# Optimization experiments

Measured on AMD Instinct MI355X. Metric: run time of the kernel, lower is better.

## Reference

```python
import jax, jax.numpy as jnp
import numpy as np

N, DIN, H, NCLS = 1024, 128, 64, 40
NEG = -1e30  # stand-in for -inf in masked max (grad-safe)


def _linw(k, fan_in, fan_out):
    s = 1.0 / np.sqrt(fan_in)
    return jax.random.uniform(k, (fan_in, fan_out), jnp.float32, -s, s)


def setup_inputs() -> dict:
    key = jax.random.key(0)
    ks = jax.random.split(key, 10)
    x = jax.random.normal(ks[0], (N, DIN), jnp.float32)
    A = jax.random.bernoulli(ks[1], 0.05, (N, N))  # bool adjacency
    D2 = 2 * H  # layer output width (concat self || neigh)
    return {
        "x": x, "A": A,
        # layer 1 (in=DIN)
        "Wp1": _linw(ks[2], DIN, DIN), "bp1": jnp.zeros((DIN,), jnp.float32),
        "Ws1": _linw(ks[3], DIN, H),   "bs1": jnp.zeros((H,), jnp.float32),
        "Wn1": _linw(ks[4], DIN, H),   "bn1": jnp.zeros((H,), jnp.float32),
        # layer 2 (in=2*H)
        "Wp2": _linw(ks[5], D2, D2),   "bp2": jnp.zeros((D2,), jnp.float32),
        "Ws2": _linw(ks[6], D2, H),    "bs2": jnp.zeros((H,), jnp.float32),
        "Wn2": _linw(ks[7], D2, H),    "bn2": jnp.zeros((H,), jnp.float32),
        # head
        "Wh": _linw(ks[8], D2, NCLS),  "bh": jnp.zeros((NCLS,), jnp.float32),
    }


def _sage_layer(x, A, Wp, bp, Ws, bs, Wn, bn):
    # maxpool aggregator: relu(Linear_pool(x_u)), elementwise max over neighbors u of v
    pooled = jax.nn.relu(x @ Wp + bp)                                  # [N, Din]
    agg = jnp.max(jnp.where(A[:, :, None], pooled[None, :, :], NEG), axis=1)  # [N, Din]
    agg = jnp.where(agg <= NEG * 0.5, 0.0, agg)                        # isolated nodes -> 0
    # out_channels = 2*hidden: concat(self transform, neighbor transform)
    return jnp.concatenate([x @ Ws + bs, agg @ Wn + bn], axis=-1)      # [N, 2H]


def _block(x, A, Wp, bp, Ws, bs, Wn, bn):
    h = jax.nn.relu(_sage_layer(x, A, Wp, bp, Ws, bs, Wn, bn))
    nrm = jnp.maximum(jnp.linalg.norm(h, axis=-1, keepdims=True), 1e-12)
    return h / nrm


def reference(x, A, Wp1, bp1, Ws1, bs1, Wn1, bn1,
              Wp2, bp2, Ws2, bs2, Wn2, bn2, Wh, bh):
    h = _block(x, A, Wp1, bp1, Ws1, bs1, Wn1, bn1)
    h = _block(h, A, Wp2, bp2, Ws2, bs2, Wn2, bn2)
    return h @ Wh + bh  # [N, n_classes]
```

## Files before the change

kernel.cpp:

```cpp
#include <hip/hip_runtime.h>

#define NN 1024

__global__ __launch_bounds__(512) void lin_build(
    const float* __restrict__ X, const float* __restrict__ Wp,
    const float* __restrict__ bp, const float* __restrict__ Ws,
    const float* __restrict__ bs, const int* __restrict__ A,
    float* __restrict__ pooled, float* __restrict__ sbuf,
    int* __restrict__ nbrG, int* __restrict__ cntG)
{
    __shared__ float xL[4][128];
    __shared__ float lp[2][4][192];
    __shared__ unsigned long long masksL[4][16];
    __shared__ int pfxL[4][16];

    const int tid  = threadIdx.x;
    const int lane = tid & 63;
    const int wv   = tid >> 6;
    const int v0   = blockIdx.x * 4;

    xL[tid >> 7][tid & 127] = X[v0 * 128 + tid];
    __syncthreads();

    if (tid < 384) {
        const int kh = (tid >= 192) ? 1 : 0;
        const int j = tid - kh * 192;
        const float* w; int ld;
        if (j < 128) { w = Wp + j;         ld = 128; }
        else         { w = Ws + (j - 128); ld = 64;  }
        const int k0 = kh * 64;
        float a0 = 0.f, a1 = 0.f, a2 = 0.f, a3 = 0.f;
        #pragma unroll 4
        for (int k = 0; k < 64; ++k) {
            const float wvv = w[(k0 + k) * ld];
            a0 += xL[0][k0 + k] * wvv;  a1 += xL[1][k0 + k] * wvv;
            a2 += xL[2][k0 + k] * wvv;  a3 += xL[3][k0 + k] * wvv;
        }
        lp[kh][0][j] = a0; lp[kh][1][j] = a1; lp[kh][2][j] = a2; lp[kh][3][j] = a3;
    }
    {
        const int r = wv >> 1;
        const int* Arow = A + (v0 + r) * NN;
        #pragma unroll
        for (int c8 = 0; c8 < 8; ++c8) {
            const int c = (wv & 1) * 8 + c8;
            const unsigned long long m = __ballot(Arow[c * 64 + lane] != 0);
            if (lane == 0) masksL[r][c] = m;
        }
    }
    __syncthreads();

    if (tid < 4) {
        int off = 0;
        #pragma unroll
        for (int c = 0; c < 16; ++c) {
            pfxL[tid][c] = off;
            off += __popcll(masksL[tid][c]);
        }
        cntG[v0 + tid] = off;
    }
    if (tid < 192) {
        #pragma unroll
        for (int r = 0; r < 4; ++r) {
            const float t = lp[0][r][tid] + lp[1][r][tid];
            if (tid < 128) pooled[(v0 + r) * 128 + tid] = fmaxf(t + bp[tid], 0.f);
            else           sbuf[(v0 + r) * 64 + (tid - 128)] = t + bs[tid - 128];
        }
    }
    __syncthreads();

    {
        const int r = wv >> 1;
        #pragma unroll
        for (int c8 = 0; c8 < 8; ++c8) {
            const int c = (wv & 1) * 8 + c8;
            const unsigned long long m = masksL[r][c];
            if ((m >> lane) & 1ull) {
                const int pos = pfxL[r][c] + __popcll(m & ((1ull << lane) - 1ull));
                nbrG[(v0 + r) * NN + pos] = c * 64 + lane;
            }
        }
    }
}

template <int MODE>
__global__ __launch_bounds__(512) void agg_kernel(
    const int* __restrict__ nbrG, const int* __restrict__ cntG,
    const float* __restrict__ pooled, const float* __restrict__ sbuf,
    const float* __restrict__ Wn, const float* __restrict__ bn,
    const float* __restrict__ Wp2, const float* __restrict__ bp2,
    const float* __restrict__ Ws2, const float* __restrict__ bs2,
    float* __restrict__ out_pooled, float* __restrict__ out_s,
    float* __restrict__ outh)
{
    __shared__ int   nbr[NN];
    __shared__ float part[4][128];
    __shared__ float aggL[128];
    __shared__ float wpart[4][64];
    __shared__ float hL[128];
    __shared__ float lpart[2][192];
    __shared__ float red[2];

    const int v   = blockIdx.x;
    const int tid = threadIdx.x;

    const int n = cntG[v];
    for (int i = tid; i < n; i += 512) nbr[i] = nbrG[v * NN + i];
    __syncthreads();

    const int d    = tid & 127;
    const int team = tid >> 7;
    float a0 = -1e30f, a1 = -1e30f, a2 = -1e30f, a3 = -1e30f;
    int p = team;
    for (; p + 12 < n; p += 16) {
        a0 = fmaxf(a0, pooled[nbr[p]      * 128 + d]);
        a1 = fmaxf(a1, pooled[nbr[p + 4]  * 128 + d]);
        a2 = fmaxf(a2, pooled[nbr[p + 8]  * 128 + d]);
        a3 = fmaxf(a3, pooled[nbr[p + 12] * 128 + d]);
    }
    for (; p < n; p += 4) a0 = fmaxf(a0, pooled[nbr[p] * 128 + d]);
    part[team][d] = fmaxf(fmaxf(a0, a1), fmaxf(a2, a3));
    __syncthreads();

    if (team == 0) {
        const float m = fmaxf(fmaxf(part[0][d], part[1][d]),
                              fmaxf(part[2][d], part[3][d]));
        aggL[d] = (m <= -5e29f) ? 0.f : m;
    }
    __syncthreads();

    if (d >= 64) {
        const int j = d - 64;
        const float* w = Wn + j;
        const int k0 = team * 32;
        float pv = 0.f;
        #pragma unroll 8
        for (int k = 0; k < 32; ++k) pv += aggL[k0 + k] * w[(k0 + k) * 64];
        wpart[team][j] = pv;
    }
    __syncthreads();

    float val = 0.f;
    if (tid < 128) {
        if (d < 64) val = sbuf[v * 64 + d];
        else {
            const int j = d - 64;
            val = bn[j] + wpart[0][j] + wpart[1][j] + wpart[2][j] + wpart[3][j];
        }
        val = fmaxf(val, 0.f);
        float ss = val * val;
        #pragma unroll
        for (int off = 32; off >= 1; off >>= 1) ss += __shfl_xor(ss, off, 64);
        if ((tid & 63) == 0) red[tid >> 6] = ss;
    }
    __syncthreads();
    if (tid < 128) {
        const float nrm = fmaxf(sqrtf(red[0] + red[1]), 1e-12f);
        hL[tid] = val / nrm;
    }
    __syncthreads();

    if (MODE == 0) {
        if (tid < 384) {
            const int kh = (tid >= 192) ? 1 : 0;
            const int j  = tid - kh * 192;
            const float* w; int ld;
            if (j < 128) { w = Wp2 + j;         ld = 128; }
            else         { w = Ws2 + (j - 128); ld = 64;  }
            float a = 0.f;
            const int k0 = kh * 64;
            #pragma unroll 4
            for (int k = 0; k < 64; ++k) a += hL[k0 + k] * w[(k0 + k) * ld];
            lpart[kh][j] = a;
        }
        __syncthreads();
        if (tid < 192) {
            const float r = lpart[0][tid] + lpart[1][tid];
            if (tid < 128) out_pooled[v * 128 + tid] = fmaxf(r + bp2[tid], 0.f);
            else           out_s[v * 64 + (tid - 128)] = r + bs2[tid - 128];
        }
    } else {
        if (tid < 64 || (tid >= 256 && tid < 320)) {
            const int kh = (tid >= 256) ? 1 : 0;
            const int j  = tid - kh * 256;
            if (j < 40) {
                float a = 0.f;
                const int k0 = kh * 64;
                #pragma unroll 4
                for (int k = 0; k < 64; ++k) a += hL[k0 + k] * Wp2[(k0 + k) * 40 + j];
                lpart[kh][j] = a;
            }
        }
        __syncthreads();
        if (tid < 40) outh[v * 40 + tid] = bp2[tid] + lpart[0][tid] + lpart[1][tid];
    }
}

extern "C" void kernel_launch(void* const* d_in, const int* in_sizes, int n_in,
                              void* d_out, int out_size, void* d_ws, size_t ws_size,
                              hipStream_t stream) {
    const float* x   = (const float*)d_in[0];
    const int*   A   = (const int*)  d_in[1];
    const float* Wp1 = (const float*)d_in[2];
    const float* bp1 = (const float*)d_in[3];
    const float* Ws1 = (const float*)d_in[4];
    const float* bs1 = (const float*)d_in[5];
    const float* Wn1 = (const float*)d_in[6];
    const float* bn1 = (const float*)d_in[7];
    const float* Wp2 = (const float*)d_in[8];
    const float* bp2 = (const float*)d_in[9];
    const float* Ws2 = (const float*)d_in[10];
    const float* bs2 = (const float*)d_in[11];
    const float* Wn2 = (const float*)d_in[12];
    const float* bn2 = (const float*)d_in[13];
    const float* Wh  = (const float*)d_in[14];
    const float* bh  = (const float*)d_in[15];
    float* out = (float*)d_out;

    char* ws = (char*)d_ws;
    float* pooled1 = (float*)(ws);
    float* s1      = (float*)(ws + (512u << 10));
    float* pooled2 = (float*)(ws + (768u << 10));
    float* s2      = (float*)(ws + (1280u << 10));
    int*   nbrG    = (int*)  (ws + (1536u << 10));
    int*   cntG    = (int*)  (ws + (5632u << 10));

    lin_build<<<NN / 4, 512, 0, stream>>>(x, Wp1, bp1, Ws1, bs1, A,
                                          pooled1, s1, nbrG, cntG);
    agg_kernel<0><<<NN, 512, 0, stream>>>(nbrG, cntG, pooled1, s1, Wn1, bn1,
                                          Wp2, bp2, Ws2, bs2,
                                          pooled2, s2, nullptr);
    agg_kernel<1><<<NN, 512, 0, stream>>>(nbrG, cntG, pooled2, s2, Wn2, bn2,
                                          Wh, bh, nullptr, nullptr,
                                          nullptr, nullptr, out);
}
```

Before: 29.71 us.

## Process two nodes per aggregation block to reuse weight loads

Each agg_kernel block now handles two nodes instead of one, halving the grid. Weight rows of Wn, Wp2/Ws2 and the head are loaded once and applied to both nodes' vectors, and the small matmuls are re-split across all 512 threads with 8-way k-partitioning. The neighbor max loop gives two thread groups to each node with 8 independent accumulators. Fewer blocks cuts per-block fixed overhead and weight traffic, at the cost of less parallelism across the GPU and imbalance when the two nodes' degrees differ.

After: 28.50 us, median of 2. -4.1%, faster.

```diff
diff --git a/kernel.cpp b/kernel.cpp
--- a/kernel.cpp
+++ b/kernel.cpp
@@ -93,70 +93,92 @@
     float* __restrict__ out_pooled, float* __restrict__ out_s,
     float* __restrict__ outh)
 {
-    __shared__ int   nbr[NN];
+    __shared__ int   nbr[2][NN];
+    __shared__ float sL[2][64];
     __shared__ float part[4][128];
-    __shared__ float aggL[128];
-    __shared__ float wpart[4][64];
-    __shared__ float hL[128];
-    __shared__ float lpart[2][192];
-    __shared__ float red[2];
-
-    const int v   = blockIdx.x;
+    __shared__ float aggL[2][128];
+    __shared__ float wq[2][8][64];
+    __shared__ float hL[2][128];
+    __shared__ float lp2[2][2][192];
+    __shared__ float red[2][2];
+
+    const int v0  = blockIdx.x * 2;
     const int tid = threadIdx.x;
 
-    const int n = cntG[v];
-    for (int i = tid; i < n; i += 512) nbr[i] = nbrG[v * NN + i];
-    __syncthreads();
-
-    const int d    = tid & 127;
-    const int team = tid >> 7;
-    float a0 = -1e30f, a1 = -1e30f, a2 = -1e30f, a3 = -1e30f;
-    int p = team;
-    for (; p + 12 < n; p += 16) {
-        a0 = fmaxf(a0, pooled[nbr[p]      * 128 + d]);
-        a1 = fmaxf(a1, pooled[nbr[p + 4]  * 128 + d]);
-        a2 = fmaxf(a2, pooled[nbr[p + 8]  * 128 + d]);
-        a3 = fmaxf(a3, pooled[nbr[p + 12] * 128 + d]);
-    }
-    for (; p < n; p += 4) a0 = fmaxf(a0, pooled[nbr[p] * 128 + d]);
-    part[team][d] = fmaxf(fmaxf(a0, a1), fmaxf(a2, a3));
-    __syncthreads();
-
-    if (team == 0) {
-        const float m = fmaxf(fmaxf(part[0][d], part[1][d]),
-                              fmaxf(part[2][d], part[3][d]));
-        aggL[d] = (m <= -5e29f) ? 0.f : m;
-    }
-    __syncthreads();
-
-    if (d >= 64) {
-        const int j = d - 64;
-        const float* w = Wn + j;
-        const int k0 = team * 32;
-        float pv = 0.f;
-        #pragma unroll 8
-        for (int k = 0; k < 32; ++k) pv += aggL[k0 + k] * w[(k0 + k) * 64];
-        wpart[team][j] = pv;
+    const int n0 = cntG[v0], n1 = cntG[v0 + 1];
+    if (tid < 128) sL[tid >> 6][tid & 63] = sbuf[v0 * 64 + tid];
+    for (int i = tid; i < n0; i += 512) nbr[0][i] = nbrG[v0 * NN + i];
+    for (int i = tid; i < n1; i += 512) nbr[1][i] = nbrG[(v0 + 1) * NN + i];
+    __syncthreads();
+
+    {
+        const int d = tid & 127, s = tid >> 7;
+        const int r = s >> 1, o = s & 1;
+        const int n = r ? n1 : n0;
+        const int* nb = nbr[r];
+        float a0=-1e30f,a1=-1e30f,a2=-1e30f,a3=-1e30f,
+              a4=-1e30f,a5=-1e30f,a6=-1e30f,a7=-1e30f;
+        int p = o;
+        for (; p + 14 < n; p += 16) {
+            a0 = fmaxf(a0, pooled[nb[p]      * 128 + d]);
+            a1 = fmaxf(a1, pooled[nb[p + 2]  * 128 + d]);
+            a2 = fmaxf(a2, pooled[nb[p + 4]  * 128 + d]);
+            a3 = fmaxf(a3, pooled[nb[p + 6]  * 128 + d]);
+            a4 = fmaxf(a4, pooled[nb[p + 8]  * 128 + d]);
+            a5 = fmaxf(a5, pooled[nb[p + 10] * 128 + d]);
+            a6 = fmaxf(a6, pooled[nb[p + 12] * 128 + d]);
+            a7 = fmaxf(a7, pooled[nb[p + 14] * 128 + d]);
+        }
+        for (; p < n; p += 2) a0 = fmaxf(a0, pooled[nb[p] * 128 + d]);
+        a0 = fmaxf(a0, a1); a2 = fmaxf(a2, a3);
+        a4 = fmaxf(a4, a5); a6 = fmaxf(a6, a7);
+        part[s][d] = fmaxf(fmaxf(a0, a2), fmaxf(a4, a6));
+    }
+    __syncthreads();
+    if (tid < 256) {
+        const int r = tid >> 7, d = tid & 127;
+        const float m = fmaxf(part[2 * r][d], part[2 * r + 1][d]);
+        aggL[r][d] = (m <= -5e29f) ? 0.f : m;
+    }
+    __syncthreads();
+
+    {
+        const int t = tid >> 6, j = tid & 63, k0 = t * 16;
+        float a0 = 0.f, a1 = 0.f;
+        #pragma unroll
+        for (int k = 0; k < 16; ++k) {
+            const float w = Wn[(k0 + k) * 64 + j];
+            a0 += aggL[0][k0 + k] * w;
+            a1 += aggL[1][k0 + k] * w;
+        }
+        wq[0][t][j] = a0; wq[1][t][j] = a1;
     }
     __syncthreads();
 
     float val = 0.f;
-    if (tid < 128) {
-        if (d < 64) val = sbuf[v * 64 + d];
-        else {
-            const int j = d - 64;
-            val = bn[j] + wpart[0][j] + wpart[1][j] + wpart[2][j] + wpart[3][j];
-        }
-        val = fmaxf(val, 0.f);
+    {
+        const int r = (tid >> 7) & 1, d = tid & 127;
+        if (tid < 256) {
+            if (d < 64) val = sL[r][d];
+            else {
+                const int j = d - 64;
+                float acc = bn[j];
+                #pragma unroll
+                for (int t = 0; t < 8; ++t) acc += wq[r][t][j];
+                val = acc;
+            }
+            val = fmaxf(val, 0.f);
+        }
         float ss = val * val;
         #pragma unroll
         for (int off = 32; off >= 1; off >>= 1) ss += __shfl_xor(ss, off, 64);
-        if ((tid & 63) == 0) red[tid >> 6] = ss;
-    }
-    __syncthreads();
-    if (tid < 128) {
-        const float nrm = fmaxf(sqrtf(red[0] + red[1]), 1e-12f);
-        hL[tid] = val / nrm;
+        if (tid < 256 && (tid & 63) == 0) red[r][(tid >> 6) & 1] = ss;
+    }
+    __syncthreads();
+    if (tid < 256) {
+        const int r = tid >> 7, d = tid & 127;
+        const float nrm = fmaxf(sqrtf(red[r][0] + red[r][1]), 1e-12f);
+        hL[r][d] = val / nrm;
     }
     __syncthreads();
 
@@ -167,32 +189,46 @@
             const float* w; int ld;
             if (j < 128) { w = Wp2 + j;         ld = 128; }
             else         { w = Ws2 + (j - 128); ld = 64;  }
-            float a = 0.f;
             const int k0 = kh * 64;
+            float a0 = 0.f, a1 = 0.f;
             #pragma unroll 4
-            for (int k = 0; k < 64; ++k) a += hL[k0 + k] * w[(k0 + k) * ld];
-            lpart[kh][j] = a;
+            for (int k = 0; k < 64; ++k) {
+                const float wv = w[(k0 + k) * ld];
+                a0 += hL[0][k0 + k] * wv;
+                a1 += hL[1][k0 + k] * wv;
+            }
+            lp2[kh][0][j] = a0; lp2[kh][1][j] = a1;
         }
         __syncthreads();
         if (tid < 192) {
-            const float r = lpart[0][tid] + lpart[1][tid];
-            if (tid < 128) out_pooled[v * 128 + tid] = fmaxf(r + bp2[tid], 0.f);
-            else           out_s[v * 64 + (tid - 128)] = r + bs2[tid - 128];
+            #pragma unroll
+            for (int r = 0; r < 2; ++r) {
+                const float t = lp2[0][r][tid] + lp2[1][r][tid];
+                if (tid < 128) out_pooled[(v0 + r) * 128 + tid] = fmaxf(t + bp2[tid], 0.f);
+                else           out_s[(v0 + r) * 64 + (tid - 128)] = t + bs2[tid - 128];
+            }
         }
     } else {
-        if (tid < 64 || (tid >= 256 && tid < 320)) {
-            const int kh = (tid >= 256) ? 1 : 0;
-            const int j  = tid - kh * 256;
-            if (j < 40) {
-                float a = 0.f;
-                const int k0 = kh * 64;
-                #pragma unroll 4
-                for (int k = 0; k < 64; ++k) a += hL[k0 + k] * Wp2[(k0 + k) * 40 + j];
-                lpart[kh][j] = a;
-            }
+        if (tid < 320) {
+            const int t = tid / 40, j = tid - t * 40;
+            const int k0 = t * 16;
+            float a0 = 0.f, a1 = 0.f;
+            #pragma unroll
+            for (int k = 0; k < 16; ++k) {
+                const float wv = Wp2[(k0 + k) * 40 + j];
+                a0 += hL[0][k0 + k] * wv;
+                a1 += hL[1][k0 + k] * wv;
+            }
+            wq[0][t][j] = a0; wq[1][t][j] = a1;
         }
         __syncthreads();
-        if (tid < 40) outh[v * 40 + tid] = bp2[tid] + lpart[0][tid] + lpart[1][tid];
+        if (tid < 80) {
+            const int r = tid / 40, j = tid - r * 40;
+            float acc = bp2[j];
+            #pragma unroll
+            for (int t = 0; t < 8; ++t) acc += wq[r][t][j];
+            outh[(v0 + r) * 40 + j] = acc;
+        }
     }
 }
 
@@ -227,10 +263,10 @@
 
     lin_build<<<NN / 4, 512, 0, stream>>>(x, Wp1, bp1, Ws1, bs1, A,
                                           pooled1, s1, nbrG, cntG);
-    agg_kernel<0><<<NN, 512, 0, stream>>>(nbrG, cntG, pooled1, s1, Wn1, bn1,
-                                          Wp2, bp2, Ws2, bs2,
-                                          pooled2, s2, nullptr);
-    agg_kernel<1><<<NN, 512, 0, stream>>>(nbrG, cntG, pooled2, s2, Wn2, bn2,
-                                          Wh, bh, nullptr, nullptr,
-                                          nullptr, nullptr, out);
+    agg_kernel<0><<<NN / 2, 512, 0, stream>>>(nbrG, cntG, pooled1, s1, Wn1, bn1,
+                                              Wp2, bp2, Ws2, bs2,
+                                              pooled2, s2, nullptr);
+    agg_kernel<1><<<NN / 2, 512, 0, stream>>>(nbrG, cntG, pooled2, s2, Wn2, bn2,
+                                              Wh, bh, nullptr, nullptr,
+                                              nullptr, nullptr, out);
 }
```

## Replace 512-thread per-node aggregation with single-wave kernel handling two nodes

Applied to the files above, without the earlier changes.

The aggregation kernels move from one 512-thread block per node to one 64-lane wavefront per block covering two nodes. Each lane gathers a float2 of pooled features with an 8-way unrolled max, and the weight matrices are read once and shared across both nodes. Most block-level syncs and cross-team shared reductions disappear in favour of wave shuffles, cutting per-node launch and sync overhead and halving weight traffic. The trade-off is much less parallelism per node, so long serial dot-product loops per lane, and neighbor lists over 256 fall back to global reads.

Result: slower. 40.39 us (+35.9%).

```diff
diff --git a/kernel.cpp b/kernel.cpp
--- a/kernel.cpp
+++ b/kernel.cpp
@@ -84,115 +84,150 @@
 }
 
 template <int MODE>
-__global__ __launch_bounds__(512) void agg_kernel(
+__global__ __launch_bounds__(64) void wave_agg(
     const int* __restrict__ nbrG, const int* __restrict__ cntG,
     const float* __restrict__ pooled, const float* __restrict__ sbuf,
     const float* __restrict__ Wn, const float* __restrict__ bn,
     const float* __restrict__ Wp2, const float* __restrict__ bp2,
     const float* __restrict__ Ws2, const float* __restrict__ bs2,
     float* __restrict__ out_pooled, float* __restrict__ out_s,
+    const float* __restrict__ Wh, const float* __restrict__ bh,
     float* __restrict__ outh)
 {
-    __shared__ int   nbr[NN];
-    __shared__ float part[4][128];
-    __shared__ float aggL[128];
-    __shared__ float wpart[4][64];
-    __shared__ float hL[128];
-    __shared__ float lpart[2][192];
-    __shared__ float red[2];
-
-    const int v   = blockIdx.x;
-    const int tid = threadIdx.x;
-
-    const int n = cntG[v];
-    for (int i = tid; i < n; i += 512) nbr[i] = nbrG[v * NN + i];
-    __syncthreads();
-
-    const int d    = tid & 127;
-    const int team = tid >> 7;
-    float a0 = -1e30f, a1 = -1e30f, a2 = -1e30f, a3 = -1e30f;
-    int p = team;
-    for (; p + 12 < n; p += 16) {
-        a0 = fmaxf(a0, pooled[nbr[p]      * 128 + d]);
-        a1 = fmaxf(a1, pooled[nbr[p + 4]  * 128 + d]);
-        a2 = fmaxf(a2, pooled[nbr[p + 8]  * 128 + d]);
-        a3 = fmaxf(a3, pooled[nbr[p + 12] * 128 + d]);
-    }
-    for (; p < n; p += 4) a0 = fmaxf(a0, pooled[nbr[p] * 128 + d]);
-    part[team][d] = fmaxf(fmaxf(a0, a1), fmaxf(a2, a3));
-    __syncthreads();
-
-    if (team == 0) {
-        const float m = fmaxf(fmaxf(part[0][d], part[1][d]),
-                              fmaxf(part[2][d], part[3][d]));
-        aggL[d] = (m <= -5e29f) ? 0.f : m;
-    }
-    __syncthreads();
-
-    if (d >= 64) {
-        const int j = d - 64;
-        const float* w = Wn + j;
-        const int k0 = team * 32;
-        float pv = 0.f;
-        #pragma unroll 8
-        for (int k = 0; k < 32; ++k) pv += aggL[k0 + k] * w[(k0 + k) * 64];
-        wpart[team][j] = pv;
-    }
-    __syncthreads();
-
-    float val = 0.f;
-    if (tid < 128) {
-        if (d < 64) val = sbuf[v * 64 + d];
-        else {
-            const int j = d - 64;
-            val = bn[j] + wpart[0][j] + wpart[1][j] + wpart[2][j] + wpart[3][j];
-        }
-        val = fmaxf(val, 0.f);
-        float ss = val * val;
-        #pragma unroll
-        for (int off = 32; off >= 1; off >>= 1) ss += __shfl_xor(ss, off, 64);
-        if ((tid & 63) == 0) red[tid >> 6] = ss;
-    }
-    __syncthreads();
-    if (tid < 128) {
-        const float nrm = fmaxf(sqrtf(red[0] + red[1]), 1e-12f);
-        hL[tid] = val / nrm;
-    }
+    __shared__ int   nbrL[2][256];
+    __shared__ float aggL[2][128];
+    __shared__ float hLL[2][128];
+
+    const int v0   = blockIdx.x * 2;
+    const int lane = threadIdx.x;
+
+    const int n0 = cntG[v0];
+    const int n1 = cntG[v0 + 1];
+    const float sv0 = sbuf[v0 * 64 + lane];
+    const float sv1 = sbuf[(v0 + 1) * 64 + lane];
+
+    for (int i = lane; i < n0 && i < 256; i += 64) nbrL[0][i] = nbrG[v0 * NN + i];
+    for (int i = lane; i < n1 && i < 256; i += 64) nbrL[1][i] = nbrG[(v0 + 1) * NN + i];
+    __syncthreads();
+
+    #pragma unroll
+    for (int r = 0; r < 2; ++r) {
+        const int n  = r ? n1 : n0;
+        const int nl = n < 256 ? n : 256;
+        const float* base = pooled + 2 * lane;
+        float2 m0 = {-1e30f, -1e30f}, m1 = m0, m2 = m0, m3 = m0;
+        float2 m4 = m0, m5 = m0, m6 = m0, m7 = m0;
+        int p = 0;
+        for (; p + 7 < nl; p += 8) {
+            const float2 t0 = *(const float2*)&base[nbrL[r][p + 0] * 128];
+            const float2 t1 = *(const float2*)&base[nbrL[r][p + 1] * 128];
+            const float2 t2 = *(const float2*)&base[nbrL[r][p + 2] * 128];
+            const float2 t3 = *(const float2*)&base[nbrL[r][p + 3] * 128];
+            const float2 t4 = *(const float2*)&base[nbrL[r][p + 4] * 128];
+            const float2 t5 = *(const float2*)&base[nbrL[r][p + 5] * 128];
+            const float2 t6 = *(const float2*)&base[nbrL[r][p + 6] * 128];
+            const float2 t7 = *(const float2*)&base[nbrL[r][p + 7] * 128];
+            m0.x = fmaxf(m0.x, t0.x); m0.y = fmaxf(m0.y, t0.y);
+            m1.x = fmaxf(m1.x, t1.x); m1.y = fmaxf(m1.y, t1.y);
+            m2.x = fmaxf(m2.x, t2.x); m2.y = fmaxf(m2.y, t2.y);
+            m3.x = fmaxf(m3.x, t3.x); m3.y = fmaxf(m3.y, t3.y);
+            m4.x = fmaxf(m4.x, t4.x); m4.y = fmaxf(m4.y, t4.y);
+            m5.x = fmaxf(m5.x, t5.x); m5.y = fmaxf(m5.y, t5.y);
+            m6.x = fmaxf(m6.x, t6.x); m6.y = fmaxf(m6.y, t6.y);
+            m7.x = fmaxf(m7.x, t7.x); m7.y = fmaxf(m7.y, t7.y);
+        }
+        for (; p < nl; ++p) {
+            const float2 t = *(const float2*)&base[nbrL[r][p] * 128];
+            m0.x = fmaxf(m0.x, t.x); m0.y = fmaxf(m0.y, t.y);
+        }
+        for (; p < n; ++p) {
+            const float2 t = *(const float2*)&base[nbrG[(v0 + r) * NN + p] * 128];
+            m0.x = fmaxf(m0.x, t.x); m0.y = fmaxf(m0.y, t.y);
+        }
+        m0.x = fmaxf(fmaxf(m0.x, m1.x), fmaxf(m2.x, m3.x));
+        m0.y = fmaxf(fmaxf(m0.y, m1.y), fmaxf(m2.y, m3.y));
+        m4.x = fmaxf(fmaxf(m4.x, m5.x), fmaxf(m6.x, m7.x));
+        m4.y = fmaxf(fmaxf(m4.y, m5.y), fmaxf(m6.y, m7.y));
+        m0.x = fmaxf(m0.x, m4.x);
+        m0.y = fmaxf(m0.y, m4.y);
+        aggL[r][2 * lane]     = (m0.x <= -5e29f) ? 0.f : m0.x;
+        aggL[r][2 * lane + 1] = (m0.y <= -5e29f) ? 0.f : m0.y;
+    }
+    __syncthreads();
+
+    float wa0 = 0.f, wa1 = 0.f;
+    #pragma unroll 4
+    for (int k4 = 0; k4 < 128; k4 += 4) {
+        const float4 g0 = *(const float4*)&aggL[0][k4];
+        const float4 g1 = *(const float4*)&aggL[1][k4];
+        const float w0 = Wn[(k4 + 0) * 64 + lane];
+        const float w1 = Wn[(k4 + 1) * 64 + lane];
+        const float w2 = Wn[(k4 + 2) * 64 + lane];
+        const float w3 = Wn[(k4 + 3) * 64 + lane];
+        wa0 += g0.x * w0 + g0.y * w1 + g0.z * w2 + g0.w * w3;
+        wa1 += g1.x * w0 + g1.y * w1 + g1.z * w2 + g1.w * w3;
+    }
+
+    const float bnj = bn[lane];
+    const float vs0 = fmaxf(sv0, 0.f), vw0 = fmaxf(wa0 + bnj, 0.f);
+    const float vs1 = fmaxf(sv1, 0.f), vw1 = fmaxf(wa1 + bnj, 0.f);
+    float ss0 = vs0 * vs0 + vw0 * vw0;
+    float ss1 = vs1 * vs1 + vw1 * vw1;
+    #pragma unroll
+    for (int off = 32; off >= 1; off >>= 1) {
+        ss0 += __shfl_xor(ss0, off, 64);
+        ss1 += __shfl_xor(ss1, off, 64);
+    }
+    const float nr0 = fmaxf(sqrtf(ss0), 1e-12f);
+    const float nr1 = fmaxf(sqrtf(ss1), 1e-12f);
+    hLL[0][lane] = vs0 / nr0;  hLL[0][64 + lane] = vw0 / nr0;
+    hLL[1][lane] = vs1 / nr1;  hLL[1][64 + lane] = vw1 / nr1;
     __syncthreads();
 
     if (MODE == 0) {
-        if (tid < 384) {
-            const int kh = (tid >= 192) ? 1 : 0;
-            const int j  = tid - kh * 192;
-            const float* w; int ld;
-            if (j < 128) { w = Wp2 + j;         ld = 128; }
-            else         { w = Ws2 + (j - 128); ld = 64;  }
-            float a = 0.f;
-            const int k0 = kh * 64;
+        float pa0 = 0.f, pb0 = 0.f, sa0 = 0.f;
+        float pa1 = 0.f, pb1 = 0.f, sa1 = 0.f;
+        #pragma unroll 4
+        for (int k4 = 0; k4 < 128; k4 += 4) {
+            const float4 h0 = *(const float4*)&hLL[0][k4];
+            const float4 h1 = *(const float4*)&hLL[1][k4];
+            #pragma unroll
+            for (int kk = 0; kk < 4; ++kk) {
+                const int k = k4 + kk;
+                const float h0k = kk == 0 ? h0.x : kk == 1 ? h0.y : kk == 2 ? h0.z : h0.w;
+                const float h1k = kk == 0 ? h1.x : kk == 1 ? h1.y : kk == 2 ? h1.z : h1.w;
+                const float wpa = Wp2[k * 128 + lane];
+                const float wpb = Wp2[k * 128 + 64 + lane];
+                const float wss = Ws2[k * 64 + lane];
+                pa0 += h0k * wpa;  pb0 += h0k * wpb;  sa0 += h0k * wss;
+                pa1 += h1k * wpa;  pb1 += h1k * wpb;  sa1 += h1k * wss;
+            }
+        }
+        const float bpa = bp2[lane], bpb = bp2[64 + lane], bss = bs2[lane];
+        out_pooled[v0 * 128 + lane]            = fmaxf(pa0 + bpa, 0.f);
+        out_pooled[v0 * 128 + 64 + lane]       = fmaxf(pb0 + bpb, 0.f);
+        out_pooled[(v0 + 1) * 128 + lane]      = fmaxf(pa1 + bpa, 0.f);
+        out_pooled[(v0 + 1) * 128 + 64 + lane] = fmaxf(pb1 + bpb, 0.f);
+        out_s[v0 * 64 + lane]       = sa0 + bss;
+        out_s[(v0 + 1) * 64 + lane] = sa1 + bss;
+    } else {
+        if (lane < 40) {
+            float a0 = 0.f, a1 = 0.f;
             #pragma unroll 4
-            for (int k = 0; k < 64; ++k) a += hL[k0 + k] * w[(k0 + k) * ld];
-            lpart[kh][j] = a;
-        }
-        __syncthreads();
-        if (tid < 192) {
-            const float r = lpart[0][tid] + lpart[1][tid];
-            if (tid < 128) out_pooled[v * 128 + tid] = fmaxf(r + bp2[tid], 0.f);
-            else           out_s[v * 64 + (tid - 128)] = r + bs2[tid - 128];
-        }
-    } else {
-        if (tid < 64 || (tid >= 256 && tid < 320)) {
-            const int kh = (tid >= 256) ? 1 : 0;
-            const int j  = tid - kh * 256;
-            if (j < 40) {
-                float a = 0.f;
-                const int k0 = kh * 64;
-                #pragma unroll 4
-                for (int k = 0; k < 64; ++k) a += hL[k0 + k] * Wp2[(k0 + k) * 40 + j];
-                lpart[kh][j] = a;
+            for (int k4 = 0; k4 < 128; k4 += 4) {
+                const float4 h0 = *(const float4*)&hLL[0][k4];
+                const float4 h1 = *(const float4*)&hLL[1][k4];
+                const float w0 = Wh[(k4 + 0) * 40 + lane];
+                const float w1 = Wh[(k4 + 1) * 40 + lane];
+                const float w2 = Wh[(k4 + 2) * 40 + lane];
+                const float w3 = Wh[(k4 + 3) * 40 + lane];
+                a0 += h0.x * w0 + h0.y * w1 + h0.z * w2 + h0.w * w3;
+                a1 += h1.x * w0 + h1.y * w1 + h1.z * w2 + h1.w * w3;
             }
-        }
-        __syncthreads();
-        if (tid < 40) outh[v * 40 + tid] = bp2[tid] + lpart[0][tid] + lpart[1][tid];
+            const float b = bh[lane];
+            outh[v0 * 40 + lane]       = b + a0;
+            outh[(v0 + 1) * 40 + lane] = b + a1;
+        }
     }
 }
 
@@ -227,10 +262,10 @@
 
     lin_build<<<NN / 4, 512, 0, stream>>>(x, Wp1, bp1, Ws1, bs1, A,
                                           pooled1, s1, nbrG, cntG);
-    agg_kernel<0><<<NN, 512, 0, stream>>>(nbrG, cntG, pooled1, s1, Wn1, bn1,
-                                          Wp2, bp2, Ws2, bs2,
-                                          pooled2, s2, nullptr);
-    agg_kernel<1><<<NN, 512, 0, stream>>>(nbrG, cntG, pooled2, s2, Wn2, bn2,
-                                          Wh, bh, nullptr, nullptr,
-                                          nullptr, nullptr, out);
+    wave_agg<0><<<NN / 2, 64, 0, stream>>>(nbrG, cntG, pooled1, s1, Wn1, bn1,
+                                           Wp2, bp2, Ws2, bs2,
+                                           pooled2, s2, nullptr, nullptr, nullptr);
+    wave_agg<1><<<NN / 2, 64, 0, stream>>>(nbrG, cntG, pooled2, s2, Wn2, bn2,
+                                           nullptr, nullptr, nullptr, nullptr,
+                                           nullptr, nullptr, Wh, bh, out);
 }
```

## Shrink aggregation blocks to 256 threads and read neighbor list directly

Applied to the files above, without the earlier changes.

The aggregation kernel now runs with 256 threads per node instead of 512. It drops the shared-memory staging of the neighbor index list and its barrier, reading indices straight from global memory in an 8-way unrolled max loop split over two halves. The layer-2 projection is no longer K-split, and the head matvec is split into four K-chunks with its own Wh/bh parameters. The goal is less synchronization and shared memory per block and higher occupancy, at the cost of fewer threads per node and possibly more global index loads.

Measured after the change: 31.70 us. 6.7% more time.

```diff
diff --git a/kernel.cpp b/kernel.cpp
--- a/kernel.cpp
+++ b/kernel.cpp
@@ -84,69 +84,73 @@
 }
 
 template <int MODE>
-__global__ __launch_bounds__(512) void agg_kernel(
+__global__ __launch_bounds__(256) void agg_kernel(
     const int* __restrict__ nbrG, const int* __restrict__ cntG,
     const float* __restrict__ pooled, const float* __restrict__ sbuf,
     const float* __restrict__ Wn, const float* __restrict__ bn,
     const float* __restrict__ Wp2, const float* __restrict__ bp2,
     const float* __restrict__ Ws2, const float* __restrict__ bs2,
     float* __restrict__ out_pooled, float* __restrict__ out_s,
+    const float* __restrict__ Wh, const float* __restrict__ bh,
     float* __restrict__ outh)
 {
-    __shared__ int   nbr[NN];
-    __shared__ float part[4][128];
+    __shared__ float part[2][128];
     __shared__ float aggL[128];
-    __shared__ float wpart[4][64];
+    __shared__ float wq[4][64];
     __shared__ float hL[128];
-    __shared__ float lpart[2][192];
     __shared__ float red[2];
 
-    const int v   = blockIdx.x;
-    const int tid = threadIdx.x;
+    const int v    = blockIdx.x;
+    const int tid  = threadIdx.x;
+    const int d    = tid & 127;
+    const int half = tid >> 7;
 
     const int n = cntG[v];
-    for (int i = tid; i < n; i += 512) nbr[i] = nbrG[v * NN + i];
-    __syncthreads();
-
-    const int d    = tid & 127;
-    const int team = tid >> 7;
-    float a0 = -1e30f, a1 = -1e30f, a2 = -1e30f, a3 = -1e30f;
-    int p = team;
-    for (; p + 12 < n; p += 16) {
-        a0 = fmaxf(a0, pooled[nbr[p]      * 128 + d]);
-        a1 = fmaxf(a1, pooled[nbr[p + 4]  * 128 + d]);
-        a2 = fmaxf(a2, pooled[nbr[p + 8]  * 128 + d]);
-        a3 = fmaxf(a3, pooled[nbr[p + 12] * 128 + d]);
-    }
-    for (; p < n; p += 4) a0 = fmaxf(a0, pooled[nbr[p] * 128 + d]);
-    part[team][d] = fmaxf(fmaxf(a0, a1), fmaxf(a2, a3));
-    __syncthreads();
-
-    if (team == 0) {
-        const float m = fmaxf(fmaxf(part[0][d], part[1][d]),
-                              fmaxf(part[2][d], part[3][d]));
+    const int* __restrict__ nb = nbrG + v * NN;
+    const float sv = (tid < 64) ? sbuf[v * 64 + tid] : 0.f;
+
+    {
+        float a0=-1e30f,a1=-1e30f,a2=-1e30f,a3=-1e30f,
+              a4=-1e30f,a5=-1e30f,a6=-1e30f,a7=-1e30f;
+        int p = half;
+        for (; p + 14 < n; p += 16) {
+            const int i0 = nb[p],      i1 = nb[p + 2],  i2 = nb[p + 4],  i3 = nb[p + 6];
+            const int i4 = nb[p + 8],  i5 = nb[p + 10], i6 = nb[p + 12], i7 = nb[p + 14];
+            a0 = fmaxf(a0, pooled[i0 * 128 + d]);
+            a1 = fmaxf(a1, pooled[i1 * 128 + d]);
+            a2 = fmaxf(a2, pooled[i2 * 128 + d]);
+            a3 = fmaxf(a3, pooled[i3 * 128 + d]);
+            a4 = fmaxf(a4, pooled[i4 * 128 + d]);
+            a5 = fmaxf(a5, pooled[i5 * 128 + d]);
+            a6 = fmaxf(a6, pooled[i6 * 128 + d]);
+            a7 = fmaxf(a7, pooled[i7 * 128 + d]);
+        }
+        for (; p < n; p += 2) a0 = fmaxf(a0, pooled[nb[p] * 128 + d]);
+        a0 = fmaxf(fmaxf(a0, a1), fmaxf(a2, a3));
+        a4 = fmaxf(fmaxf(a4, a5), fmaxf(a6, a7));
+        part[half][d] = fmaxf(a0, a4);
+    }
+    __syncthreads();
+    if (half == 0) {
+        const float m = fmaxf(part[0][d], part[1][d]);
         aggL[d] = (m <= -5e29f) ? 0.f : m;
     }
     __syncthreads();
 
-    if (d >= 64) {
-        const int j = d - 64;
-        const float* w = Wn + j;
-        const int k0 = team * 32;
-        float pv = 0.f;
+    {
+        const int j = tid & 63, kh = tid >> 6, k0 = kh * 32;
+        float a = 0.f;
         #pragma unroll 8
-        for (int k = 0; k < 32; ++k) pv += aggL[k0 + k] * w[(k0 + k) * 64];
-        wpart[team][j] = pv;
+        for (int k = 0; k < 32; ++k) a += aggL[k0 + k] * Wn[(k0 + k) * 64 + j];
+        wq[kh][j] = a;
     }
     __syncthreads();
 
     float val = 0.f;
     if (tid < 128) {
-        if (d < 64) val = sbuf[v * 64 + d];
-        else {
-            const int j = d - 64;
-            val = bn[j] + wpart[0][j] + wpart[1][j] + wpart[2][j] + wpart[3][j];
-        }
+        val = (d < 64) ? sv
+                       : (bn[d - 64] + wq[0][d - 64] + wq[1][d - 64]
+                                     + wq[2][d - 64] + wq[3][d - 64]);
         val = fmaxf(val, 0.f);
         float ss = val * val;
         #pragma unroll
@@ -161,38 +165,28 @@
     __syncthreads();
 
     if (MODE == 0) {
-        if (tid < 384) {
-            const int kh = (tid >= 192) ? 1 : 0;
-            const int j  = tid - kh * 192;
+        if (tid < 192) {
             const float* w; int ld;
-            if (j < 128) { w = Wp2 + j;         ld = 128; }
-            else         { w = Ws2 + (j - 128); ld = 64;  }
+            if (tid < 128) { w = Wp2 + tid;         ld = 128; }
+            else           { w = Ws2 + (tid - 128); ld = 64;  }
             float a = 0.f;
-            const int k0 = kh * 64;
             #pragma unroll 4
-            for (int k = 0; k < 64; ++k) a += hL[k0 + k] * w[(k0 + k) * ld];
-            lpart[kh][j] = a;
+            for (int k = 0; k < 128; ++k) a += hL[k] * w[k * ld];
+            if (tid < 128) out_pooled[v * 128 + tid] = fmaxf(a + bp2[tid], 0.f);
+            else           out_s[v * 64 + (tid - 128)] = a + bs2[tid - 128];
+        }
+    } else {
+        if (tid < 160) {
+            const int t = tid / 40, j = tid - t * 40, k0 = t * 32;
+            float a = 0.f;
+            #pragma unroll 8
+            for (int k = 0; k < 32; ++k) a += hL[k0 + k] * Wh[(k0 + k) * 40 + j];
+            wq[t][j] = a;
         }
         __syncthreads();
-        if (tid < 192) {
-            const float r = lpart[0][tid] + lpart[1][tid];
-            if (tid < 128) out_pooled[v * 128 + tid] = fmaxf(r + bp2[tid], 0.f);
-            else           out_s[v * 64 + (tid - 128)] = r + bs2[tid - 128];
-        }
-    } else {
-        if (tid < 64 || (tid >= 256 && tid < 320)) {
-            const int kh = (tid >= 256) ? 1 : 0;
-            const int j  = tid - kh * 256;
-            if (j < 40) {
-                float a = 0.f;
-                const int k0 = kh * 64;
-                #pragma unroll 4
-                for (int k = 0; k < 64; ++k) a += hL[k0 + k] * Wp2[(k0 + k) * 40 + j];
-                lpart[kh][j] = a;
-            }
-        }
-        __syncthreads();
-        if (tid < 40) outh[v * 40 + tid] = bp2[tid] + lpart[0][tid] + lpart[1][tid];
+        if (tid < 40)
+            outh[v * 40 + tid] = bh[tid] + wq[0][tid] + wq[1][tid]
+                                         + wq[2][tid] + wq[3][tid];
     }
 }
 
@@ -227,10 +221,10 @@
 
     lin_build<<<NN / 4, 512, 0, stream>>>(x, Wp1, bp1, Ws1, bs1, A,
                                           pooled1, s1, nbrG, cntG);
-    agg_kernel<0><<<NN, 512, 0, stream>>>(nbrG, cntG, pooled1, s1, Wn1, bn1,
+    agg_kernel<0><<<NN, 256, 0, stream>>>(nbrG, cntG, pooled1, s1, Wn1, bn1,
                                           Wp2, bp2, Ws2, bs2,
-                                          pooled2, s2, nullptr);
-    agg_kernel<1><<<NN, 512, 0, stream>>>(nbrG, cntG, pooled2, s2, Wn2, bn2,
-                                          Wh, bh, nullptr, nullptr,
-                                          nullptr, nullptr, out);
+                                          pooled2, s2, nullptr, nullptr, nullptr);
+    agg_kernel<1><<<NN, 256, 0, stream>>>(nbrG, cntG, pooled2, s2, Wn2, bn2,
+                                          nullptr, nullptr, nullptr, nullptr,
+                                          nullptr, nullptr, Wh, bh, out);
 }
```
